# Kernel optimization log

Measured on AMD Instinct MI355X. Metric: run time of the kernel, lower is better.

## Reference

```python
import jax, jax.numpy as jnp
import numpy as np

B = 1048576  # batch
H = 64       # rnn_hid_units


def _lstm_final(x, Wih, Whh, bih, bhh):
    """Single-layer LSTM over x: [T, B, 1]; returns final (h, c), each [B, H].
    PyTorch gate order: i, f, g, o."""
    Bn = x.shape[1]
    Hd = Whh.shape[1]
    b = bih + bhh  # fuse both bias vectors
    h0 = jnp.zeros((Bn, Hd), x.dtype)
    c0 = jnp.zeros((Bn, Hd), x.dtype)

    def step(carry, xt):
        h, c = carry
        gates = xt @ Wih.T + h @ Whh.T + b  # [B, 4H]
        i, f, g, o = jnp.split(gates, 4, axis=-1)
        i = jax.nn.sigmoid(i)
        f = jax.nn.sigmoid(f)
        g = jnp.tanh(g)
        o = jax.nn.sigmoid(o)
        c = f * c + i * g
        h = o * jnp.tanh(c)
        return (h, c), None

    (h, c), _ = jax.lax.scan(step, (h0, c0), x)
    return h, c


def setup_inputs() -> dict:
    key = jax.random.key(0)
    ks = jax.random.split(key, 18)

    def rn(k, shape, s=0.1):
        return jax.random.normal(k, shape, dtype=jnp.float32) * s

    inp = {
        "inputs": jax.random.normal(ks[0], (B, 18), dtype=jnp.float32),
        # encoder1 (nn.LSTM(1, H), single layer)
        "Wih1": rn(ks[1], (4 * H, 1)),
        "Whh1": rn(ks[2], (4 * H, H)),
        "bih1": rn(ks[3], (4 * H,)),
        "bhh1": rn(ks[4], (4 * H,)),
        # encoder2
        "Wih2": rn(ks[5], (4 * H, 1)),
        "Whh2": rn(ks[6], (4 * H, H)),
        "bih2": rn(ks[7], (4 * H,)),
        "bhh2": rn(ks[8], (4 * H,)),
        # MLP feat_trans: 2 -> 64 -> 64 -> 32 (ReLU between, linear output)
        "mW0": rn(ks[9], (64, 2)),
        "mb0": rn(ks[10], (64,)),
        "mW1": rn(ks[11], (64, 64)),
        "mb1": rn(ks[12], (64,)),
        "mW2": rn(ks[13], (32, 64)),
        "mb2": rn(ks[14], (32,)),
        # projector: 4H + 32 = 288 -> 2
        "pW": rn(ks[15], (2, 4 * H + 32)),
        "pb": rn(ks[16], (2,)),
    }
    return inp


def reference(inputs, Wih1, Whh1, bih1, bhh1, Wih2, Whh2, bih2, bhh2,
              mW0, mb0, mW1, mb1, mW2, mb2, pW, pb):
    # split_with_sizes([8, 8, 2], dim=-1)
    seq1 = inputs[:, :8].T[:, :, None]    # [8, B, 1]
    seq2 = inputs[:, 8:16].T[:, :, None]  # [8, B, 1]
    feat = inputs[:, 16:]                 # [B, 2]

    h1, c1 = _lstm_final(seq1, Wih1, Whh1, bih1, bhh1)  # [B, H] each
    h2, c2 = _lstm_final(seq2, Wih2, Whh2, bih2, bhh2)

    hid = jax.nn.relu(feat @ mW0.T + mb0)
    hid = jax.nn.relu(hid @ mW1.T + mb1)
    hid = hid @ mW2.T + mb2  # [B, 32]

    z = jnp.concatenate([h1, c1, h2, c2, hid], axis=-1)  # [B, 4H+32]
    return z @ pW.T + pb
```

## Files before the change

### kernel.cpp

```cpp
#include <hip/hip_runtime.h>

#define BLOCK 256
#define HROW 72

typedef _Float16 half_t;
typedef __attribute__((ext_vector_type(8))) _Float16 half8;
typedef __attribute__((ext_vector_type(4))) float float4v;

#define L2E  1.4426950408889634f
#define L2E2 2.8853900817779268f

__device__ __forceinline__ float rcp_(float x) { return __builtin_amdgcn_rcpf(x); }
__device__ __forceinline__ float ex2(float x)  { return __builtin_amdgcn_exp2f(x); }

extern "C" __global__ void __launch_bounds__(BLOCK, 1) mlp_kernel(
    const float* __restrict__ inputs,
    const float* __restrict__ mW0, const float* __restrict__ mb0,
    const float* __restrict__ mW1, const float* __restrict__ mb1,
    const float* __restrict__ mW2, const float* __restrict__ mb2,
    const float* __restrict__ pW, const float* __restrict__ pb,
    float* __restrict__ out, int n)
{
    int b = blockIdx.x * BLOCK + threadIdx.x;
    if (b >= n) return;
    float f0 = inputs[(size_t)b * 18 + 16], f1 = inputs[(size_t)b * 18 + 17];
    float h0[64];
    #pragma unroll
    for (int i = 0; i < 64; ++i)
        h0[i] = fmaxf(fmaf(mW0[2 * i], f0, fmaf(mW0[2 * i + 1], f1, mb0[i])), 0.0f);
    float acc2[32];
    #pragma unroll
    for (int j = 0; j < 32; ++j) acc2[j] = mb2[j];
    #pragma unroll 2
    for (int i = 0; i < 64; ++i) {
        float a = mb1[i];
        #pragma unroll
        for (int k = 0; k < 64; ++k) a = fmaf(mW1[i * 64 + k], h0[k], a);
        a = fmaxf(a, 0.0f);
        #pragma unroll
        for (int j = 0; j < 32; ++j) acc2[j] = fmaf(mW2[j * 64 + i], a, acc2[j]);
    }
    float out0 = pb[0], out1 = pb[1];
    #pragma unroll
    for (int j = 0; j < 32; ++j) {
        out0 = fmaf(pW[256 + j], acc2[j], out0);
        out1 = fmaf(pW[288 + 256 + j], acc2[j], out1);
    }
    ((float2*)out)[b] = make_float2(out0, out1);
}

template <bool LAST>
__device__ __forceinline__ void lstm_step(
    const float* __restrict__ xt,
    const half_t* __restrict__ src, half_t* __restrict__ dst,
    const half8 Bf[4][2], const float wih_v[4], const float bias_v[4],
    int l15, int quad, int jcol,
    float4v cst[4],
    const float* __restrict__ pWz,
    float* __restrict__ wpw)
{
    float ph0, pc0, ph1, pc1;
    if (LAST) {
        ph0 = pWz[jcol];       pc0 = pWz[64 + jcol];
        ph1 = pWz[288 + jcol]; pc1 = pWz[288 + 64 + jcol];
    }
    #pragma unroll
    for (int mt = 0; mt < 4; ++mt) {
        float4v x4 = *(const float4v*)&xt[mt * 16 + quad * 4];
        half8 a0 = *(const half8*)&src[(mt * 16 + l15) * HROW + quad * 8];
        half8 a1 = *(const half8*)&src[(mt * 16 + l15) * HROW + 32 + quad * 8];
        float4v ag[4];
        #pragma unroll
        for (int gg = 0; gg < 4; ++gg) {
            float4v ai;
            #pragma unroll
            for (int reg = 0; reg < 4; ++reg) ai[reg] = fmaf(x4[reg], wih_v[gg], bias_v[gg]);
            ai = __builtin_amdgcn_mfma_f32_16x16x32_f16(a0, Bf[gg][0], ai, 0, 0, 0);
            ai = __builtin_amdgcn_mfma_f32_16x16x32_f16(a1, Bf[gg][1], ai, 0, 0, 0);
            ag[gg] = ai;
        }
        float po0[4], po1[4];
        #pragma unroll
        for (int reg = 0; reg < 4; ++reg) {
            float Bi  = ex2(ag[0][reg]);
            float Bff = ex2(ag[1][reg]);
            float Bg  = ex2(ag[2][reg]);
            float Bo  = ex2(ag[3][reg]);
            float ig  = fmaf(Bi, Bg, -Bi) * rcp_((1.0f + Bi) * (1.0f + Bg));
            float cn  = fmaf(Bff * rcp_(1.0f + Bff), cst[mt][reg], ig);
            cst[mt][reg] = cn;
            float Cc  = ex2(cn * L2E2);
            float hv  = fmaf(Bo, Cc, -Bo) * rcp_((1.0f + Bo) * (1.0f + Cc));
            if (LAST) {
                po0[reg] = fmaf(ph0, hv, pc0 * cn);
                po1[reg] = fmaf(ph1, hv, pc1 * cn);
            } else {
                dst[(mt * 16 + quad * 4 + reg) * HROW + jcol] = (half_t)hv;
            }
        }
        if (LAST) {
            #pragma unroll
            for (int reg = 0; reg < 4; ++reg) {
                #pragma unroll
                for (int s = 1; s < 16; s <<= 1) {
                    po0[reg] += __shfl_xor(po0[reg], s, 64);
                    po1[reg] += __shfl_xor(po1[reg], s, 64);
                }
            }
            if (l15 == 0) {
                #pragma unroll
                for (int reg = 0; reg < 4; ++reg) {
                    int m = mt * 16 + quad * 4 + reg;
                    wpw[m * 2]     += po0[reg];
                    wpw[m * 2 + 1] += po1[reg];
                }
            }
        }
    }
    __syncthreads();
}

__device__ __forceinline__ void lstm_mfma_one(
    const float* __restrict__ Wih, const float* __restrict__ Whh,
    const float* __restrict__ bih, const float* __restrict__ bhh,
    const float* __restrict__ pW, int zbase,
    const float* __restrict__ xt,
    half_t* __restrict__ hbuf,
    int w, int lane,
    float* __restrict__ wpw)
{
    const int l15  = lane & 15;
    const int quad = lane >> 4;
    const int jcol = w * 16 + l15;

    const float gscale[4] = {L2E, L2E, L2E2, L2E};
    half8 Bf[4][2];
    float wih_v[4], bias_v[4];
    #pragma unroll
    for (int gg = 0; gg < 4; ++gg) {
        const int nrow = gg * 64 + jcol;
        const float s = gscale[gg];
        #pragma unroll
        for (int kf = 0; kf < 2; ++kf) {
            const float4* p = (const float4*)(Whh + nrow * 64 + kf * 32 + quad * 8);
            float4 w0 = p[0], w1 = p[1];
            Bf[gg][kf] = half8{(half_t)(w0.x * s), (half_t)(w0.y * s), (half_t)(w0.z * s), (half_t)(w0.w * s),
                               (half_t)(w1.x * s), (half_t)(w1.y * s), (half_t)(w1.z * s), (half_t)(w1.w * s)};
        }
        wih_v[gg]  = Wih[nrow] * s;
        bias_v[gg] = (bih[nrow] + bhh[nrow]) * s;
    }

    float4v cst[4];

    #pragma unroll
    for (int mt = 0; mt < 4; ++mt) {
        float4v x4 = *(const float4v*)&xt[mt * 16 + quad * 4];
        #pragma unroll
        for (int reg = 0; reg < 4; ++reg) {
            float Bi = ex2(fmaf(x4[reg], wih_v[0], bias_v[0]));
            float Bg = ex2(fmaf(x4[reg], wih_v[2], bias_v[2]));
            float Bo = ex2(fmaf(x4[reg], wih_v[3], bias_v[3]));
            float cn = fmaf(Bi, Bg, -Bi) * rcp_((1.0f + Bi) * (1.0f + Bg));
            cst[mt][reg] = cn;
            float Cc = ex2(cn * L2E2);
            float hv = fmaf(Bo, Cc, -Bo) * rcp_((1.0f + Bo) * (1.0f + Cc));
            hbuf[(mt * 16 + quad * 4 + reg) * HROW + jcol] = (half_t)hv;
        }
    }
    __syncthreads();

    half_t* b0 = hbuf;
    half_t* b1 = hbuf + 64 * HROW;
    #pragma unroll 1
    for (int tt = 1; tt < 7; tt += 2) {
        lstm_step<false>(xt + tt * 64,       b0, b1, Bf, wih_v, bias_v, l15, quad, jcol,
                         cst, pW, wpw);
        lstm_step<false>(xt + (tt + 1) * 64, b1, b0, Bf, wih_v, bias_v, l15, quad, jcol,
                         cst, pW, wpw);
    }
    lstm_step<true>(xt + 7 * 64, b0, b1, Bf, wih_v, bias_v, l15, quad, jcol,
                    cst, pW + zbase, wpw);
}

extern "C" __global__ void __launch_bounds__(BLOCK, 2) lstm_mfma(
    const float* __restrict__ inputs,
    const float* __restrict__ Wih1, const float* __restrict__ Whh1,
    const float* __restrict__ bih1, const float* __restrict__ bhh1,
    const float* __restrict__ Wih2, const float* __restrict__ Whh2,
    const float* __restrict__ bih2, const float* __restrict__ bhh2,
    const float* __restrict__ pW,
    float* __restrict__ out, int n)
{
    __shared__ half_t hbuf[2 * 64 * HROW];
    __shared__ float  xt_lds[16 * 64];
    __shared__ float  wp[4][64][2];

    const int tid  = threadIdx.x;
    const int w    = tid >> 6;
    const int lane = tid & 63;
    const int base = blockIdx.x * 64;

    ((float2*)wp)[tid] = make_float2(0.0f, 0.0f);
    for (int idx = tid; idx < 64 * 18; idx += BLOCK) {
        int row = idx / 18, c = idx % 18;
        float v = inputs[(size_t)(base + row) * 18 + c];
        if (c < 16) xt_lds[c * 64 + row] = v;
    }
    __syncthreads();

    float* wpw = &wp[w][0][0];
    lstm_mfma_one(Wih1, Whh1, bih1, bhh1, pW, 0,   xt_lds,          hbuf, w, lane, wpw);
    lstm_mfma_one(Wih2, Whh2, bih2, bhh2, pW, 128, xt_lds + 8 * 64, hbuf, w, lane, wpw);

    if (tid < 64) {
        int gb = base + tid;
        float2 o = ((float2*)out)[gb];
        o.x += wp[0][tid][0] + wp[1][tid][0] + wp[2][tid][0] + wp[3][tid][0];
        o.y += wp[0][tid][1] + wp[1][tid][1] + wp[2][tid][1] + wp[3][tid][1];
        ((float2*)out)[gb] = o;
    }
}

extern "C" void kernel_launch(void* const* d_in, const int* in_sizes, int n_in,
                              void* d_out, int out_size, void* d_ws, size_t ws_size,
                              hipStream_t stream) {
    const int n = in_sizes[0] / 18;
    mlp_kernel<<<(n + BLOCK - 1) / BLOCK, BLOCK, 0, stream>>>(
        (const float*)d_in[0],
        (const float*)d_in[9],  (const float*)d_in[10],
        (const float*)d_in[11], (const float*)d_in[12],
        (const float*)d_in[13], (const float*)d_in[14],
        (const float*)d_in[15], (const float*)d_in[16],
        (float*)d_out, n);
    lstm_mfma<<<n / 64, BLOCK, 0, stream>>>(
        (const float*)d_in[0],
        (const float*)d_in[1], (const float*)d_in[2],
        (const float*)d_in[3], (const float*)d_in[4],
        (const float*)d_in[5], (const float*)d_in[6],
        (const float*)d_in[7], (const float*)d_in[8],
        (const float*)d_in[15],
        (float*)d_out, n);
}
```

Baseline: 1.625 ms.

## Fuse MLP and LSTM kernels into one grid with atomics, halve LSTM tile rows

Merges the separate MLP and LSTM kernels into one launch in which every ninth block runs the MLP for 256 rows and the other eight blocks each run both LSTMs on 32 rows. Outputs are accumulated with atomicAdd after a zeroing kernel, so the two paths can overlap on the GPU instead of running back to back. The LSTM tile shrinks from 64 to 32 rows and the occupancy hint rises to 4 blocks per CU. The cost is an extra zeroing launch, atomic traffic to the output, and the MLP blocks being register-heavy while sharing the launch bounds of the LSTM blocks.

```diff
diff --git a/kernel.cpp b/kernel.cpp
--- a/kernel.cpp
+++ b/kernel.cpp
@@ -1,6 +1,7 @@
 #include <hip/hip_runtime.h>
 
 #define BLOCK 256
+#define ROWS 32
 #define HROW 72
 
 typedef _Float16 half_t;
@@ -13,40 +14,9 @@
 __device__ __forceinline__ float rcp_(float x) { return __builtin_amdgcn_rcpf(x); }
 __device__ __forceinline__ float ex2(float x)  { return __builtin_amdgcn_exp2f(x); }
 
-extern "C" __global__ void __launch_bounds__(BLOCK, 1) mlp_kernel(
-    const float* __restrict__ inputs,
-    const float* __restrict__ mW0, const float* __restrict__ mb0,
-    const float* __restrict__ mW1, const float* __restrict__ mb1,
-    const float* __restrict__ mW2, const float* __restrict__ mb2,
-    const float* __restrict__ pW, const float* __restrict__ pb,
-    float* __restrict__ out, int n)
-{
-    int b = blockIdx.x * BLOCK + threadIdx.x;
-    if (b >= n) return;
-    float f0 = inputs[(size_t)b * 18 + 16], f1 = inputs[(size_t)b * 18 + 17];
-    float h0[64];
-    #pragma unroll
-    for (int i = 0; i < 64; ++i)
-        h0[i] = fmaxf(fmaf(mW0[2 * i], f0, fmaf(mW0[2 * i + 1], f1, mb0[i])), 0.0f);
-    float acc2[32];
-    #pragma unroll
-    for (int j = 0; j < 32; ++j) acc2[j] = mb2[j];
-    #pragma unroll 2
-    for (int i = 0; i < 64; ++i) {
-        float a = mb1[i];
-        #pragma unroll
-        for (int k = 0; k < 64; ++k) a = fmaf(mW1[i * 64 + k], h0[k], a);
-        a = fmaxf(a, 0.0f);
-        #pragma unroll
-        for (int j = 0; j < 32; ++j) acc2[j] = fmaf(mW2[j * 64 + i], a, acc2[j]);
-    }
-    float out0 = pb[0], out1 = pb[1];
-    #pragma unroll
-    for (int j = 0; j < 32; ++j) {
-        out0 = fmaf(pW[256 + j], acc2[j], out0);
-        out1 = fmaf(pW[288 + 256 + j], acc2[j], out1);
-    }
-    ((float2*)out)[b] = make_float2(out0, out1);
+extern "C" __global__ void zero_out(float2* __restrict__ out, int n) {
+    int i = blockIdx.x * BLOCK + threadIdx.x;
+    if (i < n) out[i] = make_float2(0.0f, 0.0f);
 }
 
 template <bool LAST>
@@ -55,7 +25,7 @@
     const half_t* __restrict__ src, half_t* __restrict__ dst,
     const half8 Bf[4][2], const float wih_v[4], const float bias_v[4],
     int l15, int quad, int jcol,
-    float4v cst[4],
+    float4v cst[2],
     const float* __restrict__ pWz,
     float* __restrict__ wpw)
 {
@@ -65,7 +35,7 @@
         ph1 = pWz[288 + jcol]; pc1 = pWz[288 + 64 + jcol];
     }
     #pragma unroll
-    for (int mt = 0; mt < 4; ++mt) {
+    for (int mt = 0; mt < 2; ++mt) {
         float4v x4 = *(const float4v*)&xt[mt * 16 + quad * 4];
         half8 a0 = *(const half8*)&src[(mt * 16 + l15) * HROW + quad * 8];
         half8 a1 = *(const half8*)&src[(mt * 16 + l15) * HROW + 32 + quad * 8];
@@ -151,10 +121,10 @@
         bias_v[gg] = (bih[nrow] + bhh[nrow]) * s;
     }
 
-    float4v cst[4];
+    float4v cst[2];
 
     #pragma unroll
-    for (int mt = 0; mt < 4; ++mt) {
+    for (int mt = 0; mt < 2; ++mt) {
         float4v x4 = *(const float4v*)&xt[mt * 16 + quad * 4];
         #pragma unroll
         for (int reg = 0; reg < 4; ++reg) {
@@ -171,54 +141,95 @@
     __syncthreads();
 
     half_t* b0 = hbuf;
-    half_t* b1 = hbuf + 64 * HROW;
+    half_t* b1 = hbuf + ROWS * HROW;
     #pragma unroll 1
     for (int tt = 1; tt < 7; tt += 2) {
-        lstm_step<false>(xt + tt * 64,       b0, b1, Bf, wih_v, bias_v, l15, quad, jcol,
+        lstm_step<false>(xt + tt * ROWS,       b0, b1, Bf, wih_v, bias_v, l15, quad, jcol,
                          cst, pW, wpw);
-        lstm_step<false>(xt + (tt + 1) * 64, b1, b0, Bf, wih_v, bias_v, l15, quad, jcol,
+        lstm_step<false>(xt + (tt + 1) * ROWS, b1, b0, Bf, wih_v, bias_v, l15, quad, jcol,
                          cst, pW, wpw);
     }
-    lstm_step<true>(xt + 7 * 64, b0, b1, Bf, wih_v, bias_v, l15, quad, jcol,
+    lstm_step<true>(xt + 7 * ROWS, b0, b1, Bf, wih_v, bias_v, l15, quad, jcol,
                     cst, pW + zbase, wpw);
 }
 
-extern "C" __global__ void __launch_bounds__(BLOCK, 2) lstm_mfma(
+extern "C" __global__ void __launch_bounds__(BLOCK, 4) fused_kernel(
     const float* __restrict__ inputs,
     const float* __restrict__ Wih1, const float* __restrict__ Whh1,
     const float* __restrict__ bih1, const float* __restrict__ bhh1,
     const float* __restrict__ Wih2, const float* __restrict__ Whh2,
     const float* __restrict__ bih2, const float* __restrict__ bhh2,
-    const float* __restrict__ pW,
+    const float* __restrict__ mW0, const float* __restrict__ mb0,
+    const float* __restrict__ mW1, const float* __restrict__ mb1,
+    const float* __restrict__ mW2, const float* __restrict__ mb2,
+    const float* __restrict__ pW, const float* __restrict__ pb,
     float* __restrict__ out, int n)
 {
-    __shared__ half_t hbuf[2 * 64 * HROW];
-    __shared__ float  xt_lds[16 * 64];
-    __shared__ float  wp[4][64][2];
+    const int g = blockIdx.x / 9;
+    const int r = blockIdx.x % 9;
+
+    if (r == 8) {
+        int b = g * BLOCK + (int)threadIdx.x;
+        if (b < n) {
+            float f0 = inputs[(size_t)b * 18 + 16], f1 = inputs[(size_t)b * 18 + 17];
+            float h0[64];
+            #pragma unroll
+            for (int i = 0; i < 64; ++i)
+                h0[i] = fmaxf(fmaf(mW0[2 * i], f0, fmaf(mW0[2 * i + 1], f1, mb0[i])), 0.0f);
+            float acc2[32];
+            #pragma unroll
+            for (int j = 0; j < 32; ++j) acc2[j] = mb2[j];
+            #pragma unroll 2
+            for (int i = 0; i < 64; ++i) {
+                float a = mb1[i];
+                #pragma unroll
+                for (int k = 0; k < 64; ++k) a = fmaf(mW1[i * 64 + k], h0[k], a);
+                a = fmaxf(a, 0.0f);
+                #pragma unroll
+                for (int j = 0; j < 32; ++j) acc2[j] = fmaf(mW2[j * 64 + i], a, acc2[j]);
+            }
+            float out0 = pb[0], out1 = pb[1];
+            #pragma unroll
+            for (int j = 0; j < 32; ++j) {
+                out0 = fmaf(pW[256 + j], acc2[j], out0);
+                out1 = fmaf(pW[288 + 256 + j], acc2[j], out1);
+            }
+            atomicAdd(&out[2 * (size_t)b],     out0);
+            atomicAdd(&out[2 * (size_t)b + 1], out1);
+        }
+        return;
+    }
+
+    const int lb = g * 8 + r;
+    if (lb * ROWS >= n) return;
+
+    __shared__ half_t hbuf[2 * ROWS * HROW];
+    __shared__ float  xt_lds[16 * ROWS];
+    __shared__ float  wp[4][ROWS][2];
 
     const int tid  = threadIdx.x;
     const int w    = tid >> 6;
     const int lane = tid & 63;
-    const int base = blockIdx.x * 64;
-
-    ((float2*)wp)[tid] = make_float2(0.0f, 0.0f);
-    for (int idx = tid; idx < 64 * 18; idx += BLOCK) {
+    const int base = lb * ROWS;
+
+    ((float*)wp)[tid] = 0.0f;
+    for (int idx = tid; idx < ROWS * 18; idx += BLOCK) {
         int row = idx / 18, c = idx % 18;
         float v = inputs[(size_t)(base + row) * 18 + c];
-        if (c < 16) xt_lds[c * 64 + row] = v;
+        if (c < 16) xt_lds[c * ROWS + row] = v;
     }
     __syncthreads();
 
     float* wpw = &wp[w][0][0];
-    lstm_mfma_one(Wih1, Whh1, bih1, bhh1, pW, 0,   xt_lds,          hbuf, w, lane, wpw);
-    lstm_mfma_one(Wih2, Whh2, bih2, bhh2, pW, 128, xt_lds + 8 * 64, hbuf, w, lane, wpw);
-
-    if (tid < 64) {
+    lstm_mfma_one(Wih1, Whh1, bih1, bhh1, pW, 0,   xt_lds,            hbuf, w, lane, wpw);
+    lstm_mfma_one(Wih2, Whh2, bih2, bhh2, pW, 128, xt_lds + 8 * ROWS, hbuf, w, lane, wpw);
+
+    if (tid < ROWS) {
         int gb = base + tid;
-        float2 o = ((float2*)out)[gb];
-        o.x += wp[0][tid][0] + wp[1][tid][0] + wp[2][tid][0] + wp[3][tid][0];
-        o.y += wp[0][tid][1] + wp[1][tid][1] + wp[2][tid][1] + wp[3][tid][1];
-        ((float2*)out)[gb] = o;
+        float sx = wp[0][tid][0] + wp[1][tid][0] + wp[2][tid][0] + wp[3][tid][0];
+        float sy = wp[0][tid][1] + wp[1][tid][1] + wp[2][tid][1] + wp[3][tid][1];
+        atomicAdd(&out[2 * (size_t)gb],     sx);
+        atomicAdd(&out[2 * (size_t)gb + 1], sy);
     }
 }
 
@@ -226,19 +237,19 @@
                               void* d_out, int out_size, void* d_ws, size_t ws_size,
                               hipStream_t stream) {
     const int n = in_sizes[0] / 18;
-    mlp_kernel<<<(n + BLOCK - 1) / BLOCK, BLOCK, 0, stream>>>(
+    const int nmlp = (n + BLOCK - 1) / BLOCK;
+    const int ngrid = nmlp * 9;
+
+    zero_out<<<nmlp, BLOCK, 0, stream>>>((float2*)d_out, n);
+    fused_kernel<<<ngrid, BLOCK, 0, stream>>>(
         (const float*)d_in[0],
+        (const float*)d_in[1],  (const float*)d_in[2],
+        (const float*)d_in[3],  (const float*)d_in[4],
+        (const float*)d_in[5],  (const float*)d_in[6],
+        (const float*)d_in[7],  (const float*)d_in[8],
         (const float*)d_in[9],  (const float*)d_in[10],
         (const float*)d_in[11], (const float*)d_in[12],
         (const float*)d_in[13], (const float*)d_in[14],
         (const float*)d_in[15], (const float*)d_in[16],
         (float*)d_out, n);
-    lstm_mfma<<<n / 64, BLOCK, 0, stream>>>(
-        (const float*)d_in[0],
-        (const float*)d_in[1], (const float*)d_in[2],
-        (const float*)d_in[3], (const float*)d_in[4],
-        (const float*)d_in[5], (const float*)d_in[6],
-        (const float*)d_in[7], (const float*)d_in[8],
-        (const float*)d_in[15],
-        (float*)d_out, n);
-}
+}
```

Result: slower. 1.761 ms (+8.4%).

## Interleave both LSTM encoders in one timestep loop to share barriers

Applied to the files above, without the earlier changes.

Runs the two independent LSTM recurrences together: each timestep now issues MFMAs and gate math for both encoders before a single barrier, using separate double-buffered hidden-state LDS buffers. This halves the number of __syncthreads and gives the scheduler independent work to hide MFMA and transcendental latency. In exchange it doubles the weight fragments and cell state held in registers and doubles hidden-state LDS, which can cut occupancy below the requested two blocks per CU or cause spills.

```diff
diff --git a/kernel.cpp b/kernel.cpp
--- a/kernel.cpp
+++ b/kernel.cpp
@@ -49,53 +49,132 @@
     ((float2*)out)[b] = make_float2(out0, out1);
 }
 
-template <bool LAST>
-__device__ __forceinline__ void lstm_step(
-    const float* __restrict__ xt,
-    const half_t* __restrict__ src, half_t* __restrict__ dst,
-    const half8 Bf[4][2], const float wih_v[4], const float bias_v[4],
-    int l15, int quad, int jcol,
-    float4v cst[4],
-    const float* __restrict__ pWz,
-    float* __restrict__ wpw)
-{
-    float ph0, pc0, ph1, pc1;
-    if (LAST) {
-        ph0 = pWz[jcol];       pc0 = pWz[64 + jcol];
-        ph1 = pWz[288 + jcol]; pc1 = pWz[288 + 64 + jcol];
-    }
+__device__ __forceinline__ void setup_weights(
+    const float* __restrict__ Wih, const float* __restrict__ Whh,
+    const float* __restrict__ bih, const float* __restrict__ bhh,
+    int quad, int jcol,
+    half8 Bf[4][2], float wih_v[4], float bias_v[4])
+{
+    const float gscale[4] = {L2E, L2E, L2E2, L2E};
+    #pragma unroll
+    for (int gg = 0; gg < 4; ++gg) {
+        const int nrow = gg * 64 + jcol;
+        const float s = gscale[gg];
+        #pragma unroll
+        for (int kf = 0; kf < 2; ++kf) {
+            const float4* p = (const float4*)(Whh + nrow * 64 + kf * 32 + quad * 8);
+            float4 w0 = p[0], w1 = p[1];
+            Bf[gg][kf] = half8{(half_t)(w0.x * s), (half_t)(w0.y * s), (half_t)(w0.z * s), (half_t)(w0.w * s),
+                               (half_t)(w1.x * s), (half_t)(w1.y * s), (half_t)(w1.z * s), (half_t)(w1.w * s)};
+        }
+        wih_v[gg]  = Wih[nrow] * s;
+        bias_v[gg] = (bih[nrow] + bhh[nrow]) * s;
+    }
+}
+
+__device__ __forceinline__ void lstm_init(
+    const float* __restrict__ xt, const float wih_v[4], const float bias_v[4],
+    half_t* __restrict__ buf0, int quad, int jcol, float4v cst[4])
+{
     #pragma unroll
     for (int mt = 0; mt < 4; ++mt) {
         float4v x4 = *(const float4v*)&xt[mt * 16 + quad * 4];
-        half8 a0 = *(const half8*)&src[(mt * 16 + l15) * HROW + quad * 8];
-        half8 a1 = *(const half8*)&src[(mt * 16 + l15) * HROW + 32 + quad * 8];
-        float4v ag[4];
+        #pragma unroll
+        for (int reg = 0; reg < 4; ++reg) {
+            float Bi = ex2(fmaf(x4[reg], wih_v[0], bias_v[0]));
+            float Bg = ex2(fmaf(x4[reg], wih_v[2], bias_v[2]));
+            float Bo = ex2(fmaf(x4[reg], wih_v[3], bias_v[3]));
+            float cn = fmaf(Bi, Bg, -Bi) * rcp_((1.0f + Bi) * (1.0f + Bg));
+            cst[mt][reg] = cn;
+            float Cc = ex2(cn * L2E2);
+            float hv = fmaf(Bo, Cc, -Bo) * rcp_((1.0f + Bo) * (1.0f + Cc));
+            buf0[(mt * 16 + quad * 4 + reg) * HROW + jcol] = (half_t)hv;
+        }
+    }
+}
+
+template <bool LAST>
+__device__ __forceinline__ void lstm_step2(
+    const float* __restrict__ xtA, const float* __restrict__ xtB,
+    const half_t* __restrict__ srcA, half_t* __restrict__ dstA,
+    const half_t* __restrict__ srcB, half_t* __restrict__ dstB,
+    const half8 Bf[2][4][2], const float wih_v[2][4], const float bias_v[2][4],
+    int l15, int quad, int jcol,
+    float4v cstA[4], float4v cstB[4],
+    const float* __restrict__ pW,
+    float* __restrict__ wpw)
+{
+    float phA0, pcA0, phA1, pcA1, phB0, pcB0, phB1, pcB1;
+    if (LAST) {
+        phA0 = pW[jcol];             pcA0 = pW[64 + jcol];
+        phA1 = pW[288 + jcol];       pcA1 = pW[288 + 64 + jcol];
+        phB0 = pW[128 + jcol];       pcB0 = pW[128 + 64 + jcol];
+        phB1 = pW[288 + 128 + jcol]; pcB1 = pW[288 + 128 + 64 + jcol];
+    }
+    #pragma unroll
+    for (int mt = 0; mt < 4; ++mt) {
+        float4v x4A = *(const float4v*)&xtA[mt * 16 + quad * 4];
+        half8 a0A = *(const half8*)&srcA[(mt * 16 + l15) * HROW + quad * 8];
+        half8 a1A = *(const half8*)&srcA[(mt * 16 + l15) * HROW + 32 + quad * 8];
+        float4v agA[4];
         #pragma unroll
         for (int gg = 0; gg < 4; ++gg) {
             float4v ai;
             #pragma unroll
-            for (int reg = 0; reg < 4; ++reg) ai[reg] = fmaf(x4[reg], wih_v[gg], bias_v[gg]);
-            ai = __builtin_amdgcn_mfma_f32_16x16x32_f16(a0, Bf[gg][0], ai, 0, 0, 0);
-            ai = __builtin_amdgcn_mfma_f32_16x16x32_f16(a1, Bf[gg][1], ai, 0, 0, 0);
-            ag[gg] = ai;
-        }
+            for (int reg = 0; reg < 4; ++reg) ai[reg] = fmaf(x4A[reg], wih_v[0][gg], bias_v[0][gg]);
+            ai = __builtin_amdgcn_mfma_f32_16x16x32_f16(a0A, Bf[0][gg][0], ai, 0, 0, 0);
+            ai = __builtin_amdgcn_mfma_f32_16x16x32_f16(a1A, Bf[0][gg][1], ai, 0, 0, 0);
+            agA[gg] = ai;
+        }
+        float4v x4B = *(const float4v*)&xtB[mt * 16 + quad * 4];
+        half8 a0B = *(const half8*)&srcB[(mt * 16 + l15) * HROW + quad * 8];
+        half8 a1B = *(const half8*)&srcB[(mt * 16 + l15) * HROW + 32 + quad * 8];
+        float4v agB[4];
+        #pragma unroll
+        for (int gg = 0; gg < 4; ++gg) {
+            float4v ai;
+            #pragma unroll
+            for (int reg = 0; reg < 4; ++reg) ai[reg] = fmaf(x4B[reg], wih_v[1][gg], bias_v[1][gg]);
+            ai = __builtin_amdgcn_mfma_f32_16x16x32_f16(a0B, Bf[1][gg][0], ai, 0, 0, 0);
+            ai = __builtin_amdgcn_mfma_f32_16x16x32_f16(a1B, Bf[1][gg][1], ai, 0, 0, 0);
+            agB[gg] = ai;
+        }
+
         float po0[4], po1[4];
         #pragma unroll
         for (int reg = 0; reg < 4; ++reg) {
-            float Bi  = ex2(ag[0][reg]);
-            float Bff = ex2(ag[1][reg]);
-            float Bg  = ex2(ag[2][reg]);
-            float Bo  = ex2(ag[3][reg]);
+            float Bi  = ex2(agA[0][reg]);
+            float Bff = ex2(agA[1][reg]);
+            float Bg  = ex2(agA[2][reg]);
+            float Bo  = ex2(agA[3][reg]);
             float ig  = fmaf(Bi, Bg, -Bi) * rcp_((1.0f + Bi) * (1.0f + Bg));
-            float cn  = fmaf(Bff * rcp_(1.0f + Bff), cst[mt][reg], ig);
-            cst[mt][reg] = cn;
+            float cn  = fmaf(Bff * rcp_(1.0f + Bff), cstA[mt][reg], ig);
+            cstA[mt][reg] = cn;
             float Cc  = ex2(cn * L2E2);
             float hv  = fmaf(Bo, Cc, -Bo) * rcp_((1.0f + Bo) * (1.0f + Cc));
             if (LAST) {
-                po0[reg] = fmaf(ph0, hv, pc0 * cn);
-                po1[reg] = fmaf(ph1, hv, pc1 * cn);
+                po0[reg] = fmaf(phA0, hv, pcA0 * cn);
+                po1[reg] = fmaf(phA1, hv, pcA1 * cn);
             } else {
-                dst[(mt * 16 + quad * 4 + reg) * HROW + jcol] = (half_t)hv;
+                dstA[(mt * 16 + quad * 4 + reg) * HROW + jcol] = (half_t)hv;
+            }
+        }
+        #pragma unroll
+        for (int reg = 0; reg < 4; ++reg) {
+            float Bi  = ex2(agB[0][reg]);
+            float Bff = ex2(agB[1][reg]);
+            float Bg  = ex2(agB[2][reg]);
+            float Bo  = ex2(agB[3][reg]);
+            float ig  = fmaf(Bi, Bg, -Bi) * rcp_((1.0f + Bi) * (1.0f + Bg));
+            float cn  = fmaf(Bff * rcp_(1.0f + Bff), cstB[mt][reg], ig);
+            cstB[mt][reg] = cn;
+            float Cc  = ex2(cn * L2E2);
+            float hv  = fmaf(Bo, Cc, -Bo) * rcp_((1.0f + Bo) * (1.0f + Cc));
+            if (LAST) {
+                po0[reg] = fmaf(phB0, hv, fmaf(pcB0, cn, po0[reg]));
+                po1[reg] = fmaf(phB1, hv, fmaf(pcB1, cn, po1[reg]));
+            } else {
+                dstB[(mt * 16 + quad * 4 + reg) * HROW + jcol] = (half_t)hv;
             }
         }
         if (LAST) {
@@ -120,69 +199,6 @@
     __syncthreads();
 }
 
-__device__ __forceinline__ void lstm_mfma_one(
-    const float* __restrict__ Wih, const float* __restrict__ Whh,
-    const float* __restrict__ bih, const float* __restrict__ bhh,
-    const float* __restrict__ pW, int zbase,
-    const float* __restrict__ xt,
-    half_t* __restrict__ hbuf,
-    int w, int lane,
-    float* __restrict__ wpw)
-{
-    const int l15  = lane & 15;
-    const int quad = lane >> 4;
-    const int jcol = w * 16 + l15;
-
-    const float gscale[4] = {L2E, L2E, L2E2, L2E};
-    half8 Bf[4][2];
-    float wih_v[4], bias_v[4];
-    #pragma unroll
-    for (int gg = 0; gg < 4; ++gg) {
-        const int nrow = gg * 64 + jcol;
-        const float s = gscale[gg];
-        #pragma unroll
-        for (int kf = 0; kf < 2; ++kf) {
-            const float4* p = (const float4*)(Whh + nrow * 64 + kf * 32 + quad * 8);
-            float4 w0 = p[0], w1 = p[1];
-            Bf[gg][kf] = half8{(half_t)(w0.x * s), (half_t)(w0.y * s), (half_t)(w0.z * s), (half_t)(w0.w * s),
-                               (half_t)(w1.x * s), (half_t)(w1.y * s), (half_t)(w1.z * s), (half_t)(w1.w * s)};
-        }
-        wih_v[gg]  = Wih[nrow] * s;
-        bias_v[gg] = (bih[nrow] + bhh[nrow]) * s;
-    }
-
-    float4v cst[4];
-
-    #pragma unroll
-    for (int mt = 0; mt < 4; ++mt) {
-        float4v x4 = *(const float4v*)&xt[mt * 16 + quad * 4];
-        #pragma unroll
-        for (int reg = 0; reg < 4; ++reg) {
-            float Bi = ex2(fmaf(x4[reg], wih_v[0], bias_v[0]));
-            float Bg = ex2(fmaf(x4[reg], wih_v[2], bias_v[2]));
-            float Bo = ex2(fmaf(x4[reg], wih_v[3], bias_v[3]));
-            float cn = fmaf(Bi, Bg, -Bi) * rcp_((1.0f + Bi) * (1.0f + Bg));
-            cst[mt][reg] = cn;
-            float Cc = ex2(cn * L2E2);
-            float hv = fmaf(Bo, Cc, -Bo) * rcp_((1.0f + Bo) * (1.0f + Cc));
-            hbuf[(mt * 16 + quad * 4 + reg) * HROW + jcol] = (half_t)hv;
-        }
-    }
-    __syncthreads();
-
-    half_t* b0 = hbuf;
-    half_t* b1 = hbuf + 64 * HROW;
-    #pragma unroll 1
-    for (int tt = 1; tt < 7; tt += 2) {
-        lstm_step<false>(xt + tt * 64,       b0, b1, Bf, wih_v, bias_v, l15, quad, jcol,
-                         cst, pW, wpw);
-        lstm_step<false>(xt + (tt + 1) * 64, b1, b0, Bf, wih_v, bias_v, l15, quad, jcol,
-                         cst, pW, wpw);
-    }
-    lstm_step<true>(xt + 7 * 64, b0, b1, Bf, wih_v, bias_v, l15, quad, jcol,
-                    cst, pW + zbase, wpw);
-}
-
 extern "C" __global__ void __launch_bounds__(BLOCK, 2) lstm_mfma(
     const float* __restrict__ inputs,
     const float* __restrict__ Wih1, const float* __restrict__ Whh1,
@@ -192,7 +208,8 @@
     const float* __restrict__ pW,
     float* __restrict__ out, int n)
 {
-    __shared__ half_t hbuf[2 * 64 * HROW];
+    __shared__ half_t hbufA[2 * 64 * HROW];
+    __shared__ half_t hbufB[2 * 64 * HROW];
     __shared__ float  xt_lds[16 * 64];
     __shared__ float  wp[4][64][2];
 
@@ -200,6 +217,9 @@
     const int w    = tid >> 6;
     const int lane = tid & 63;
     const int base = blockIdx.x * 64;
+    const int l15  = lane & 15;
+    const int quad = lane >> 4;
+    const int jcol = w * 16 + l15;
 
     ((float2*)wp)[tid] = make_float2(0.0f, 0.0f);
     for (int idx = tid; idx < 64 * 18; idx += BLOCK) {
@@ -209,9 +229,32 @@
     }
     __syncthreads();
 
+    half8 Bf[2][4][2];
+    float wih_v[2][4], bias_v[2][4];
+    setup_weights(Wih1, Whh1, bih1, bhh1, quad, jcol, Bf[0], wih_v[0], bias_v[0]);
+    setup_weights(Wih2, Whh2, bih2, bhh2, quad, jcol, Bf[1], wih_v[1], bias_v[1]);
+
+    const float* xA = xt_lds;
+    const float* xB = xt_lds + 8 * 64;
+
+    float4v cstA[4], cstB[4];
+    lstm_init(xA, wih_v[0], bias_v[0], hbufA, quad, jcol, cstA);
+    lstm_init(xB, wih_v[1], bias_v[1], hbufB, quad, jcol, cstB);
+    __syncthreads();
+
     float* wpw = &wp[w][0][0];
-    lstm_mfma_one(Wih1, Whh1, bih1, bhh1, pW, 0,   xt_lds,          hbuf, w, lane, wpw);
-    lstm_mfma_one(Wih2, Whh2, bih2, bhh2, pW, 128, xt_lds + 8 * 64, hbuf, w, lane, wpw);
+    half_t* A0 = hbufA; half_t* A1 = hbufA + 64 * HROW;
+    half_t* B0 = hbufB; half_t* B1 = hbufB + 64 * HROW;
+
+    #pragma unroll 1
+    for (int tt = 1; tt < 7; tt += 2) {
+        lstm_step2<false>(xA + tt * 64,       xB + tt * 64,       A0, A1, B0, B1,
+                          Bf, wih_v, bias_v, l15, quad, jcol, cstA, cstB, pW, wpw);
+        lstm_step2<false>(xA + (tt + 1) * 64, xB + (tt + 1) * 64, A1, A0, B1, B0,
+                          Bf, wih_v, bias_v, l15, quad, jcol, cstA, cstB, pW, wpw);
+    }
+    lstm_step2<true>(xA + 7 * 64, xB + 7 * 64, A0, A1, B0, B1,
+                     Bf, wih_v, bias_v, l15, quad, jcol, cstA, cstB, pW, wpw);
 
     if (tid < 64) {
         int gb = base + tid;
```

After: 3.054 ms. 88.0% more time.

## Merge MLP and LSTM kernels into one heterogeneous grid with atomic accumulation

Applied to the files above, without the earlier changes.

Folds the scalar MLP branch into the LSTM MFMA kernel as every fifth block, so the FMA-heavy MLP work can run concurrently with the matrix-core LSTM blocks instead of in a separate serial launch. Both branches now accumulate into the output with atomicAdd, which requires a new zero-fill kernel beforehand. The merged kernel's register and launch bounds now apply to the MLP path, which may change its occupancy, and the atomics add some traffic.

```diff
diff --git a/kernel.cpp b/kernel.cpp
--- a/kernel.cpp
+++ b/kernel.cpp
@@ -13,40 +13,9 @@
 __device__ __forceinline__ float rcp_(float x) { return __builtin_amdgcn_rcpf(x); }
 __device__ __forceinline__ float ex2(float x)  { return __builtin_amdgcn_exp2f(x); }
 
-extern "C" __global__ void __launch_bounds__(BLOCK, 1) mlp_kernel(
-    const float* __restrict__ inputs,
-    const float* __restrict__ mW0, const float* __restrict__ mb0,
-    const float* __restrict__ mW1, const float* __restrict__ mb1,
-    const float* __restrict__ mW2, const float* __restrict__ mb2,
-    const float* __restrict__ pW, const float* __restrict__ pb,
-    float* __restrict__ out, int n)
-{
-    int b = blockIdx.x * BLOCK + threadIdx.x;
-    if (b >= n) return;
-    float f0 = inputs[(size_t)b * 18 + 16], f1 = inputs[(size_t)b * 18 + 17];
-    float h0[64];
-    #pragma unroll
-    for (int i = 0; i < 64; ++i)
-        h0[i] = fmaxf(fmaf(mW0[2 * i], f0, fmaf(mW0[2 * i + 1], f1, mb0[i])), 0.0f);
-    float acc2[32];
-    #pragma unroll
-    for (int j = 0; j < 32; ++j) acc2[j] = mb2[j];
-    #pragma unroll 2
-    for (int i = 0; i < 64; ++i) {
-        float a = mb1[i];
-        #pragma unroll
-        for (int k = 0; k < 64; ++k) a = fmaf(mW1[i * 64 + k], h0[k], a);
-        a = fmaxf(a, 0.0f);
-        #pragma unroll
-        for (int j = 0; j < 32; ++j) acc2[j] = fmaf(mW2[j * 64 + i], a, acc2[j]);
-    }
-    float out0 = pb[0], out1 = pb[1];
-    #pragma unroll
-    for (int j = 0; j < 32; ++j) {
-        out0 = fmaf(pW[256 + j], acc2[j], out0);
-        out1 = fmaf(pW[288 + 256 + j], acc2[j], out1);
-    }
-    ((float2*)out)[b] = make_float2(out0, out1);
+extern "C" __global__ void zero_out(float2* __restrict__ out, int n) {
+    int i = blockIdx.x * BLOCK + threadIdx.x;
+    if (i < n) out[i] = make_float2(0.0f, 0.0f);
 }
 
 template <bool LAST>
@@ -189,17 +158,56 @@
     const float* __restrict__ bih1, const float* __restrict__ bhh1,
     const float* __restrict__ Wih2, const float* __restrict__ Whh2,
     const float* __restrict__ bih2, const float* __restrict__ bhh2,
-    const float* __restrict__ pW,
+    const float* __restrict__ mW0, const float* __restrict__ mb0,
+    const float* __restrict__ mW1, const float* __restrict__ mb1,
+    const float* __restrict__ mW2, const float* __restrict__ mb2,
+    const float* __restrict__ pW, const float* __restrict__ pb,
     float* __restrict__ out, int n)
 {
     __shared__ half_t hbuf[2 * 64 * HROW];
     __shared__ float  xt_lds[16 * 64];
     __shared__ float  wp[4][64][2];
 
-    const int tid  = threadIdx.x;
+    const int g = blockIdx.x / 5;
+    const int r = blockIdx.x % 5;
+    const int tid = threadIdx.x;
+
+    if (r == 4) {
+        int b = g * BLOCK + tid;
+        if (b < n) {
+            float f0 = inputs[(size_t)b * 18 + 16], f1 = inputs[(size_t)b * 18 + 17];
+            float h0[64];
+            #pragma unroll
+            for (int i = 0; i < 64; ++i)
+                h0[i] = fmaxf(fmaf(mW0[2 * i], f0, fmaf(mW0[2 * i + 1], f1, mb0[i])), 0.0f);
+            float acc2[32];
+            #pragma unroll
+            for (int j = 0; j < 32; ++j) acc2[j] = mb2[j];
+            #pragma unroll 2
+            for (int i = 0; i < 64; ++i) {
+                float a = mb1[i];
+                #pragma unroll
+                for (int k = 0; k < 64; ++k) a = fmaf(mW1[i * 64 + k], h0[k], a);
+                a = fmaxf(a, 0.0f);
+                #pragma unroll
+                for (int j = 0; j < 32; ++j) acc2[j] = fmaf(mW2[j * 64 + i], a, acc2[j]);
+            }
+            float out0 = pb[0], out1 = pb[1];
+            #pragma unroll
+            for (int j = 0; j < 32; ++j) {
+                out0 = fmaf(pW[256 + j], acc2[j], out0);
+                out1 = fmaf(pW[288 + 256 + j], acc2[j], out1);
+            }
+            atomicAdd(&out[2 * (size_t)b],     out0);
+            atomicAdd(&out[2 * (size_t)b + 1], out1);
+        }
+        return;
+    }
+
+    const int lb   = g * 4 + r;
     const int w    = tid >> 6;
     const int lane = tid & 63;
-    const int base = blockIdx.x * 64;
+    const int base = lb * 64;
 
     ((float2*)wp)[tid] = make_float2(0.0f, 0.0f);
     for (int idx = tid; idx < 64 * 18; idx += BLOCK) {
@@ -215,10 +223,10 @@
 
     if (tid < 64) {
         int gb = base + tid;
-        float2 o = ((float2*)out)[gb];
-        o.x += wp[0][tid][0] + wp[1][tid][0] + wp[2][tid][0] + wp[3][tid][0];
-        o.y += wp[0][tid][1] + wp[1][tid][1] + wp[2][tid][1] + wp[3][tid][1];
-        ((float2*)out)[gb] = o;
+        float sx = wp[0][tid][0] + wp[1][tid][0] + wp[2][tid][0] + wp[3][tid][0];
+        float sy = wp[0][tid][1] + wp[1][tid][1] + wp[2][tid][1] + wp[3][tid][1];
+        atomicAdd(&out[2 * (size_t)gb],     sx);
+        atomicAdd(&out[2 * (size_t)gb + 1], sy);
     }
 }
 
@@ -226,19 +234,19 @@
                               void* d_out, int out_size, void* d_ws, size_t ws_size,
                               hipStream_t stream) {
     const int n = in_sizes[0] / 18;
-    mlp_kernel<<<(n + BLOCK - 1) / BLOCK, BLOCK, 0, stream>>>(
+    const int nmlp = (n + BLOCK - 1) / BLOCK;
+    const int ngrid = nmlp * 5;
+
+    zero_out<<<nmlp, BLOCK, 0, stream>>>((float2*)d_out, n);
+    lstm_mfma<<<ngrid, BLOCK, 0, stream>>>(
         (const float*)d_in[0],
+        (const float*)d_in[1],  (const float*)d_in[2],
+        (const float*)d_in[3],  (const float*)d_in[4],
+        (const float*)d_in[5],  (const float*)d_in[6],
+        (const float*)d_in[7],  (const float*)d_in[8],
         (const float*)d_in[9],  (const float*)d_in[10],
         (const float*)d_in[11], (const float*)d_in[12],
         (const float*)d_in[13], (const float*)d_in[14],
         (const float*)d_in[15], (const float*)d_in[16],
         (float*)d_out, n);
-    lstm_mfma<<<n / 64, BLOCK, 0, stream>>>(
-        (const float*)d_in[0],
-        (const float*)d_in[1], (const float*)d_in[2],
-        (const float*)d_in[3], (const float*)d_in[4],
-        (const float*)d_in[5], (const float*)d_in[6],
-        (const float*)d_in[7], (const float*)d_in[8],
-        (const float*)d_in[15],
-        (float*)d_out, n);
-}
+}
```

New measurement: 1.689 ms. +4.0%, slower.
